# Optimization experiments

Hardware: AMD Instinct MI355X
Metric: run time of the kernel (lower is better)

## Reference

```python
import jax, jax.numpy as jnp
import numpy as np

# config (mirrors init_kwargs)
R = 1.0           # ball-query radius
K = 32            # ball-query neighbors
SPATIAL_STRIDE = 4
TKS = 3           # temporal kernel size (odd)
TPAD = (1, 1)     # replicate temporal padding
HEADS = 8
DIM_HEAD = 64
DIM = 512
MLP = 2048
DEPTH = 2
LN_EPS = 1e-5


def fps(xyz, m):
    # CUDA-style furthest point sampling, starts at index 0. xyz: [N,3] -> [m] int32
    N = xyz.shape[0]
    def body(carry, _):
        dists, last = carry
        d = jnp.sum((xyz - xyz[last]) ** 2, axis=-1)
        dists = jnp.minimum(dists, d)
        nxt = jnp.argmax(dists).astype(jnp.int32)
        return (dists, nxt), nxt
    init = (jnp.full((N,), 1e10, xyz.dtype), jnp.int32(0))
    _, idxs = jax.lax.scan(body, init, None, length=m - 1)
    return jnp.concatenate([jnp.zeros((1,), jnp.int32), idxs])


def ball_query(neighbor_xyz, anchor_xyz):
    # first K neighbor indices within radius R (pad with first found, 0 if none)
    N = neighbor_xyz.shape[0]
    d2 = jnp.sum((anchor_xyz[:, None, :] - neighbor_xyz[None, :, :]) ** 2, -1)  # [M,N]
    cand = jnp.where(d2 < R * R, jnp.arange(N, dtype=jnp.int32)[None, :], N)
    firstk = jnp.sort(cand, axis=-1)[:, :K]
    first = firstk[:, :1]
    idx = jnp.where(firstk >= N, first, firstk)
    return jnp.where(idx >= N, 0, idx).astype(jnp.int32)


def layer_norm(x, g, b):
    mu = jnp.mean(x, -1, keepdims=True)
    var = jnp.var(x, -1, keepdims=True)
    return (x - mu) * jax.lax.rsqrt(var + LN_EPS) * g + b


def p4dconv(xyzs, Wd):
    # tube embedding: FPS anchors + ball-query grouping + 1x1 conv on (dx,dy,dz,dt)
    B, T, N, _ = xyzs.shape
    pad = jnp.concatenate([xyzs[:, :1]] * TPAD[0] + [xyzs] + [xyzs[:, -1:]] * TPAD[1], axis=1)
    Lp = pad.shape[1]
    m = N // SPATIAL_STRIDE
    half = TKS // 2
    new_xyzs, new_feats = [], []
    for t in range(half, Lp - half, 1):  # temporal_stride = 1
        frame = pad[:, t]                                  # [B,N,3]
        aidx = jax.vmap(lambda x: fps(x, m))(frame)        # [B,m]
        anchor = jax.vmap(lambda f, ix: f[ix])(frame, aidx)  # [B,m,3]
        feats_t = []
        for i in range(t - half, t + half + 1):
            nb = pad[:, i]                                 # [B,N,3]
            idx = jax.vmap(ball_query)(nb, anchor)         # [B,m,K]
            grouped = jax.vmap(lambda n, ix: n[ix])(nb, idx)  # [B,m,K,3]
            disp = grouped - anchor[:, :, None, :]
            tdisp = jnp.full((B, m, K, 1), float(i - t), disp.dtype)
            d4 = jnp.concatenate([disp, tdisp], -1)        # [B,m,K,4]
            f = jnp.einsum('bmkf,cf->bmkc', d4, Wd)        # 1x1 conv, no bias/BN/act
            feats_t.append(jnp.max(f, axis=2))             # spatial max pool
        new_feats.append(jnp.max(jnp.stack(feats_t, 1), axis=1))  # temporal max pool
        new_xyzs.append(anchor)
    return jnp.stack(new_xyzs, 1), jnp.stack(new_feats, 1)  # [B,L,m,3], [B,L,m,C]


def attention(xyzs, feats, Wqkv, Wsp, Wout, bout, g, b):
    B, L, n, C = feats.shape
    M = L * n
    x = layer_norm(feats, g, b)
    qkv = jnp.einsum('blnc,ec->blne', x, Wqkv).reshape(B, M, 3, HEADS, DIM_HEAD)
    q, k, v = [jnp.transpose(qkv[:, :, j], (0, 2, 1, 3)) for j in range(3)]  # [B,h,M,d]
    dots = jnp.einsum('bhid,bhjd->bhij', q, k) * (DIM_HEAD ** -0.5)
    attn = jax.nn.softmax(dots, axis=-1)
    out_v = jnp.einsum('bhij,bhjd->bhid', attn, v)
    xyz_f = xyzs.reshape(B, M, 3)
    delta = xyz_f[:, None, :, :] - xyz_f[:, :, None, :]      # [B,i,j,3] = xyz_j - xyz_i
    wdelta = jnp.einsum('bhij,bijc->bhic', attn, delta)      # attn-weighted displacement
    disp_f = jnp.einsum('bhic,dc->bhid', wdelta, Wsp)        # spatial_op Linear(3->d)
    out = out_v + disp_f
    out = jnp.transpose(out, (0, 2, 1, 3)).reshape(B, M, HEADS * DIM_HEAD)
    out = jax.nn.gelu(out @ Wout.T + bout, approximate=False)
    return out.reshape(B, L, n, C) + feats


def feed_forward(x, g, b, W1, b1, W2, b2):
    h = layer_norm(x, g, b)
    h = jax.nn.gelu(h @ W1.T + b1, approximate=False)
    return h @ W2.T + b2 + x


def setup_inputs() -> dict:
    key = jax.random.key(0)
    ks = jax.random.split(key, 12)
    s = 0.02
    inner = HEADS * DIM_HEAD
    return {
        'xyzs': jax.random.normal(ks[0], (2, 4, 1024, 3), jnp.float32),
        'Wd': jax.random.normal(ks[1], (DIM, 4), jnp.float32) * s,
        'Wqkv': jax.random.normal(ks[2], (DEPTH, 3 * inner, DIM), jnp.float32) * s,
        'Wsp': jax.random.normal(ks[3], (DEPTH, DIM_HEAD, 3), jnp.float32) * s,
        'Wout': jax.random.normal(ks[4], (DEPTH, DIM, inner), jnp.float32) * s,
        'bout': jnp.zeros((DEPTH, DIM), jnp.float32),
        'ln1_g': jnp.ones((DEPTH, DIM), jnp.float32),
        'ln1_b': jnp.zeros((DEPTH, DIM), jnp.float32),
        'Wff1': jax.random.normal(ks[5], (DEPTH, MLP, DIM), jnp.float32) * s,
        'bff1': jnp.zeros((DEPTH, MLP), jnp.float32),
        'Wff2': jax.random.normal(ks[6], (DEPTH, DIM, MLP), jnp.float32) * s,
        'bff2': jnp.zeros((DEPTH, DIM), jnp.float32),
        'ln2_g': jnp.ones((DEPTH, DIM), jnp.float32),
        'ln2_b': jnp.zeros((DEPTH, DIM), jnp.float32),
    }


def reference(xyzs, Wd, Wqkv, Wsp, Wout, bout, ln1_g, ln1_b, Wff1, bff1, Wff2, bff2, ln2_g, ln2_b):
    new_xyzs, feats = p4dconv(xyzs, Wd)   # [B,L,m,3], [B,L,m,DIM]
    feats = jax.nn.relu(feats)            # emb_relu after tube embedding
    for i in range(DEPTH):
        feats = attention(new_xyzs, feats, Wqkv[i], Wsp[i], Wout[i], bout[i], ln1_g[i], ln1_b[i])
        feats = feed_forward(feats, ln2_g[i], ln2_b[i], Wff1[i], bff1[i], Wff2[i], bff2[i])
    return feats
```

## Files before the change

kernel.cpp:

```cpp
#include <hip/hip_runtime.h>
#include <math.h>
#include <stdint.h>


typedef __bf16 bf16_t;
typedef __bf16 bf16x8 __attribute__((ext_vector_type(8)));
typedef __bf16 bf16x4 __attribute__((ext_vector_type(4)));
typedef float f32x4 __attribute__((ext_vector_type(4)));

__device__ __forceinline__ void async16(const bf16_t* g, bf16_t* l) {
  __builtin_amdgcn_global_load_lds(
      (const __attribute__((address_space(1))) void*)g,
      (__attribute__((address_space(3))) void*)l, 16, 0, 0);
}

__device__ __forceinline__ float wave_max_dpp(float v) {
  int a = __float_as_int(v);
  int t;
  t = __builtin_amdgcn_update_dpp(a, a, 0x111, 0xf, 0xf, false);
  a = __float_as_int(fmaxf(__int_as_float(a), __int_as_float(t)));
  t = __builtin_amdgcn_update_dpp(a, a, 0x112, 0xf, 0xf, false);
  a = __float_as_int(fmaxf(__int_as_float(a), __int_as_float(t)));
  t = __builtin_amdgcn_update_dpp(a, a, 0x114, 0xf, 0xf, false);
  a = __float_as_int(fmaxf(__int_as_float(a), __int_as_float(t)));
  t = __builtin_amdgcn_update_dpp(a, a, 0x118, 0xf, 0xf, false);
  a = __float_as_int(fmaxf(__int_as_float(a), __int_as_float(t)));
  t = __builtin_amdgcn_update_dpp(a, a, 0x142, 0xf, 0xf, false);
  a = __float_as_int(fmaxf(__int_as_float(a), __int_as_float(t)));
  t = __builtin_amdgcn_update_dpp(a, a, 0x143, 0xf, 0xf, false);
  a = __float_as_int(fmaxf(__int_as_float(a), __int_as_float(t)));
  return __int_as_float(a);
}

template <int CTRL>
__device__ __forceinline__ unsigned long long dpp_max_u64(unsigned long long kv) {
  uint32_t lo = (uint32_t)kv, hi = (uint32_t)(kv >> 32);
  uint32_t lo2 =
      (uint32_t)__builtin_amdgcn_update_dpp((int)lo, (int)lo, CTRL, 0xf, 0xf, false);
  uint32_t hi2 =
      (uint32_t)__builtin_amdgcn_update_dpp((int)hi, (int)hi, CTRL, 0xf, 0xf, false);
  unsigned long long other = ((unsigned long long)hi2 << 32) | lo2;
  return other > kv ? other : kv;
}

__global__ __launch_bounds__(512) void fps_cvt_kernel(
    const float* __restrict__ xyzs, float* __restrict__ anchors,
    const float* __restrict__ s0, bf16_t* __restrict__ d0,
    const float* __restrict__ s1, bf16_t* __restrict__ d1,
    const float* __restrict__ s2, bf16_t* __restrict__ d2,
    const float* __restrict__ s3, bf16_t* __restrict__ d3) {
  int bid = blockIdx.x;
  int tid = threadIdx.x;
  if (bid >= 8) {
    int idx = (bid - 8) * 512 + tid;
    const float* s; bf16_t* d; int off;
    if (idx < 393216) { s = s0; d = d0; off = idx; }
    else if (idx < 524288) { s = s1; d = d1; off = idx - 393216; }
    else if (idx < 1048576) { s = s2; d = d2; off = idx - 524288; }
    else { s = s3; d = d3; off = idx - 1048576; }
    float4 v = ((const float4*)s)[off];
    bf16x4 o = {(bf16_t)v.x, (bf16_t)v.y, (bf16_t)v.z, (bf16_t)v.w};
    ((bf16x4*)d)[off] = o;
    return;
  }
  int to = bid & 3, b = bid >> 2;
  const float* fr = xyzs + (size_t)(b * 4 + to) * 1024 * 3;
  float* an = anchors + (size_t)(b * 4 + to) * 256 * 3;
  __shared__ __align__(16) float4 sp[1024];
  __shared__ __align__(16) unsigned long long keys[2][8];
  int w = tid >> 6, lane = tid & 63;
  float px[2], py[2], pz[2], dist[2];
#pragma unroll
  for (int r = 0; r < 2; ++r) {
    int i = r * 512 + tid;
    float x = fr[i * 3 + 0], y = fr[i * 3 + 1], z = fr[i * 3 + 2];
    px[r] = x; py[r] = y; pz[r] = z; dist[r] = 1e10f;
    sp[i] = make_float4(x, y, z, 0.0f);
  }
  __syncthreads();
  float4 c = sp[0];
  if (tid == 0) { an[0] = c.x; an[1] = c.y; an[2] = c.z; }
  for (int s = 1; s < 256; ++s) {
    int par = s & 1;
#pragma unroll
    for (int r = 0; r < 2; ++r) {
      float dx = px[r] - c.x, dy = py[r] - c.y, dz = pz[r] - c.z;
      float d = fmaf(dx, dx, fmaf(dy, dy, dz * dz));
      dist[r] = fminf(dist[r], d);
    }
    float mloc = fmaxf(dist[0], dist[1]);
    float wmax = wave_max_dpp(mloc);
    float smax = __int_as_float(__builtin_amdgcn_readlane(__float_as_int(wmax), 63));
    unsigned int cidx = 0xFFFFFFFFu;
#pragma unroll
    for (int r = 1; r >= 0; --r) {
      unsigned long long m = __ballot(dist[r] == smax);
      unsigned int tz = (unsigned int)__builtin_ctzll(m | 0x8000000000000000ull);
      unsigned int cand = (unsigned int)(r * 512 + w * 64) + tz;
      cidx = m ? cand : cidx;
    }
    unsigned long long key =
        ((unsigned long long)__float_as_uint(smax) << 32) |
        (unsigned long long)(~cidx);
    if (lane == 0) keys[par][w] = key;
    __syncthreads();
    unsigned long long kv = keys[par][lane & 7];
    kv = dpp_max_u64<0xB1>(kv);
    kv = dpp_max_u64<0x4E>(kv);
    kv = dpp_max_u64<0x124>(kv);
    unsigned int bi = ~(unsigned int)(kv & 0xFFFFFFFFull);
    c = sp[bi];
    if (tid == 0) { an[s * 3 + 0] = c.x; an[s * 3 + 1] = c.y; an[s * 3 + 2] = c.z; }
  }
}

__global__ __launch_bounds__(256) void conv_ln_kernel(
    const float* __restrict__ xyzs, const float* __restrict__ anchors,
    const float* __restrict__ Wd, float* __restrict__ feats,
    bf16_t* __restrict__ xln0, const float* __restrict__ g,
    const float* __restrict__ bt) {
  int bid = blockIdx.x;
  int tid = threadIdx.x;
  int j = bid & 255, to = (bid >> 8) & 3, b = bid >> 10;
  __shared__ float disp[96][4];
  __shared__ int idxbuf[3][32];
  __shared__ float red1[4], red2[4];
  const float* an = anchors + (size_t)((b * 4 + to) * 256 + j) * 3;
  float ax = an[0], ay = an[1], az = an[2];
  int w = tid >> 6, lane = tid & 63;
  if (w < 3) {
    int src = to + w - 1; src = src < 0 ? 0 : (src > 3 ? 3 : src);
    const float* nb = xyzs + (size_t)(b * 4 + src) * 1024 * 3;
    int cnt = 0;
    for (int ch = 0; ch < 16; ++ch) {
      if (cnt >= 32) break;
      int i = ch * 64 + lane;
      float dx = ax - nb[i * 3], dy = ay - nb[i * 3 + 1], dz = az - nb[i * 3 + 2];
      float d2 = dx * dx + dy * dy + dz * dz;
      bool in = d2 < 1.0f;
      unsigned long long mask = __ballot(in);
      if (in) {
        int pos = cnt + (int)__popcll(mask & ((1ull << lane) - 1ull));
        if (pos < 32) idxbuf[w][pos] = i;
      }
      cnt += (int)__popcll(mask);
    }
    if (cnt > 32) cnt = 32;
    if (lane >= cnt && lane < 32) idxbuf[w][lane] = (cnt > 0) ? idxbuf[w][0] : 0;
    if (lane < 32) {
      int ni = idxbuf[w][lane];
      int row = w * 32 + lane;
      disp[row][0] = nb[ni * 3 + 0] - ax;
      disp[row][1] = nb[ni * 3 + 1] - ay;
      disp[row][2] = nb[ni * 3 + 2] - az;
      disp[row][3] = (float)(w - 1);
    }
  }
  __syncthreads();
  int row = (b * 1024) + to * 256 + j;
  const float* wr0 = Wd + tid * 4;
  const float* wr1 = Wd + (tid + 256) * 4;
  float w00 = wr0[0], w01 = wr0[1], w02 = wr0[2], w03 = wr0[3];
  float w10 = wr1[0], w11 = wr1[1], w12 = wr1[2], w13 = wr1[3];
  float mx0 = -1e30f, mx1 = -1e30f;
#pragma unroll 8
  for (int nn = 0; nn < 96; ++nn) {
    float a0 = disp[nn][0], a1 = disp[nn][1], a2 = disp[nn][2], a3 = disp[nn][3];
    mx0 = fmaxf(mx0, a0 * w00 + a1 * w01 + a2 * w02 + a3 * w03);
    mx1 = fmaxf(mx1, a0 * w10 + a1 * w11 + a2 * w12 + a3 * w13);
  }
  float v0 = fmaxf(mx0, 0.0f), v1 = fmaxf(mx1, 0.0f);
  float* fout = feats + (size_t)row * 512;
  fout[tid] = v0;
  fout[tid + 256] = v1;
  float s = v0 + v1;
#pragma unroll
  for (int off = 32; off >= 1; off >>= 1) s += __shfl_xor(s, off, 64);
  if (lane == 0) red1[w] = s;
  __syncthreads();
  float mu = (red1[0] + red1[1] + red1[2] + red1[3]) * (1.0f / 512.0f);
  float dd0 = v0 - mu, dd1 = v1 - mu;
  float q = dd0 * dd0 + dd1 * dd1;
#pragma unroll
  for (int off = 32; off >= 1; off >>= 1) q += __shfl_xor(q, off, 64);
  if (lane == 0) red2[w] = q;
  __syncthreads();
  float var = (red2[0] + red2[1] + red2[2] + red2[3]) * (1.0f / 512.0f);
  float rs = rsqrtf(var + 1e-5f);
  bf16_t* yr = xln0 + (size_t)row * 512;
  yr[tid] = (bf16_t)(dd0 * rs * g[tid] + bt[tid]);
  yr[tid + 256] = (bf16_t)(dd1 * rs * g[tid + 256] + bt[tid + 256]);
}

__global__ __launch_bounds__(256) void ln_kernel(
    const float* __restrict__ x, const float* __restrict__ g,
    const float* __restrict__ bt, bf16_t* __restrict__ y) {
  int row = blockIdx.x;
  int tid = threadIdx.x;
  const float* xr = x + (size_t)row * 512;
  float v0 = xr[tid], v1 = xr[tid + 256];
  float s = v0 + v1;
#pragma unroll
  for (int off = 32; off >= 1; off >>= 1) s += __shfl_xor(s, off, 64);
  __shared__ float red1[4], red2[4];
  int w = tid >> 6, lane = tid & 63;
  if (lane == 0) red1[w] = s;
  __syncthreads();
  float mu = (red1[0] + red1[1] + red1[2] + red1[3]) * (1.0f / 512.0f);
  float d0 = v0 - mu, d1 = v1 - mu;
  float q = d0 * d0 + d1 * d1;
#pragma unroll
  for (int off = 32; off >= 1; off >>= 1) q += __shfl_xor(q, off, 64);
  if (lane == 0) red2[w] = q;
  __syncthreads();
  float var = (red2[0] + red2[1] + red2[2] + red2[3]) * (1.0f / 512.0f);
  float rs = rsqrtf(var + 1e-5f);
  bf16_t* yr = y + (size_t)row * 512;
  yr[tid] = (bf16_t)(d0 * rs * g[tid] + bt[tid]);
  yr[tid + 256] = (bf16_t)(d1 * rs * g[tid + 256] + bt[tid + 256]);
}

template <int BM, int BN, bool GELU, bool BIAS, bool RES, bool OUTBF>
__global__ __launch_bounds__(256) void gemm_bf16(
    const bf16_t* __restrict__ A, const bf16_t* __restrict__ W,
    const float* __restrict__ bias, const float* __restrict__ res,
    void* __restrict__ Cout, int Mn, int Nn, int Kn) {
  constexpr int BK = 64;
  constexpr int WM = BM / 2, WN = BN / 2;
  constexpr int MT = WM / 16, NT = WN / 16;
  constexpr int AIT = (BM * BK / 8) / 256;
  constexpr int BIT = (BN * BK / 8) / 256;
  __shared__ __align__(16) bf16_t As[BM * BK];
  __shared__ __align__(16) bf16_t Bs[BN * BK];
  int tid = threadIdx.x;
  int w = tid >> 6, lane = tid & 63;
  int wr = w >> 1, wc = w & 1;
  int m0 = blockIdx.y * BM, n0 = blockIdx.x * BN;
  int l15 = lane & 15, quad = lane >> 4;
  f32x4 acc[MT][NT] = {};

  const int a_fo = (wr * WM + l15) * BK + quad * 8;
  const int b_fo = (wc * WN + l15) * BK + quad * 8;

  for (int k0 = 0; k0 < Kn; k0 += BK) {
    __syncthreads();
#pragma unroll
    for (int i = 0; i < AIT; ++i) {
      int chunk = i * 256 + tid;
      int row = chunk >> 3, c8 = chunk & 7;
      async16(A + ((size_t)(m0 + row) * Kn + k0 + c8 * 8), As + chunk * 8);
    }
#pragma unroll
    for (int i = 0; i < BIT; ++i) {
      int chunk = i * 256 + tid;
      int row = chunk >> 3, c8 = chunk & 7;
      async16(W + ((size_t)(n0 + row) * Kn + k0 + c8 * 8), Bs + chunk * 8);
    }
    __syncthreads();
#pragma unroll
    for (int ks = 0; ks < 2; ++ks) {
      bf16x8 aF[MT], bF[NT];
#pragma unroll
      for (int mt = 0; mt < MT; ++mt)
        aF[mt] = *(const bf16x8*)&As[a_fo + mt * 16 * BK + ks * 32];
#pragma unroll
      for (int nt = 0; nt < NT; ++nt)
        bF[nt] = *(const bf16x8*)&Bs[b_fo + nt * 16 * BK + ks * 32];
#pragma unroll
      for (int mt = 0; mt < MT; ++mt)
#pragma unroll
        for (int nt = 0; nt < NT; ++nt)
          acc[mt][nt] = __builtin_amdgcn_mfma_f32_16x16x32_bf16(
              aF[mt], bF[nt], acc[mt][nt], 0, 0, 0);
    }
  }
  int rbase = quad * 4;
#pragma unroll
  for (int mt = 0; mt < MT; ++mt) {
#pragma unroll
    for (int reg = 0; reg < 4; ++reg) {
      int r = m0 + wr * WM + mt * 16 + rbase + reg;
      size_t roff = (size_t)r * Nn;
#pragma unroll
      for (int nt = 0; nt < NT; ++nt) {
        int c = n0 + wc * WN + nt * 16 + l15;
        float v = acc[mt][nt][reg];
        if (BIAS) v += bias[c];
        if (GELU) v = v * 0.5f * (1.0f + erff(v * 0.7071067811865475f));
        if (RES) v += res[roff + c];
        if (OUTBF) ((bf16_t*)Cout)[roff + c] = (bf16_t)v;
        else ((float*)Cout)[roff + c] = v;
      }
    }
  }
}

__global__ __launch_bounds__(256) void attn_kernel(
    const bf16_t* __restrict__ qkv, const float* __restrict__ xyzf,
    const float* __restrict__ Wsp, bf16_t* __restrict__ outp) {
  int bid = blockIdx.x;
  int qt = bid & 15, h = (bid >> 4) & 7, b = bid >> 7;
  int tid = threadIdx.x;
  int w = tid >> 6, lane = tid & 63;
  int l15 = lane & 15, quad = lane >> 4;

  __shared__ __align__(16) bf16_t Kb[2][64 * 64];
  __shared__ __align__(16) bf16_t Vt[2][64 * 72];
  __shared__ __align__(16) bf16_t Ps[4][16 * 72];
  __shared__ __align__(16) float4 Xs[2][64];

  const size_t tokbase = (size_t)b * 1024;
  int qbase = qt * 64 + w * 16;

  bf16x8 aQ[2];
  {
    const bf16_t* qp = qkv + (tokbase + qbase + l15) * 1536 + h * 64 + quad * 8;
    aQ[0] = *(const bf16x8*)(qp);
    aQ[1] = *(const bf16x8*)(qp + 32);
  }

  f32x4 oacc[4] = {};
  float lr[4] = {}, pxr[4] = {}, pyr[4] = {}, pzr[4] = {};

  auto stage = [&](int ch, int buf) {
    int j0 = ch * 64;
    int r0 = tid >> 3, seg = tid & 7;
    const bf16_t* g0 = qkv + (tokbase + j0 + r0) * 1536 + 512 + h * 64 + seg * 8;
    async16(g0, Kb[buf] + tid * 8);
    const bf16_t* g1 = qkv + (tokbase + j0 + 32 + r0) * 1536 + 512 + h * 64 + seg * 8;
    async16(g1, Kb[buf] + 2048 + tid * 8);
#pragma unroll
    for (int t = 0; t < 4; ++t) {
      int task = t * 256 + tid;
      int rp = task >> 5, c2 = task & 31;
      const uint32_t* vsrc = (const uint32_t*)(qkv + (tokbase + j0 + 2 * rp) * 1536 +
                                               1024 + h * 64 + 2 * c2);
      uint32_t a = vsrc[0];
      uint32_t bq = vsrc[768];
      uint32_t wlo = (a & 0xffffu) | (bq << 16);
      uint32_t whi = (a >> 16) | (bq & 0xffff0000u);
      uint32_t* vd = (uint32_t*)Vt[buf];
      vd[c2 * 72 + rp] = wlo;
      vd[c2 * 72 + 36 + rp] = whi;
    }
    if (tid < 64) {
      const float* xp = xyzf + (tokbase + j0 + tid) * 3;
      Xs[buf][tid] = make_float4(xp[0], xp[1], xp[2], 0.0f);
    }
  };

  stage(0, 0);
  for (int ch = 0; ch < 16; ++ch) {
    int cur = ch & 1;
    __syncthreads();
    if (ch + 1 < 16) stage(ch + 1, cur ^ 1);
    f32x4 sacc[4] = {};
#pragma unroll
    for (int ks = 0; ks < 2; ++ks)
#pragma unroll
      for (int nt = 0; nt < 4; ++nt) {
        bf16x8 bK = *(const bf16x8*)&Kb[cur][(nt * 16 + l15) * 64 + ks * 32 + quad * 8];
        sacc[nt] = __builtin_amdgcn_mfma_f32_16x16x32_bf16(aQ[ks], bK, sacc[nt], 0, 0, 0);
      }
#pragma unroll
    for (int nt = 0; nt < 4; ++nt) {
      float4 xk = Xs[cur][nt * 16 + l15];
#pragma unroll
      for (int reg = 0; reg < 4; ++reg) {
        float p = __expf(sacc[nt][reg] * 0.125f);
        bf16_t pb = (bf16_t)p;
        float pf = (float)pb;
        Ps[w][(quad * 4 + reg) * 72 + nt * 16 + l15] = pb;
        lr[reg] += pf;
        pxr[reg] = fmaf(pf, xk.x, pxr[reg]);
        pyr[reg] = fmaf(pf, xk.y, pyr[reg]);
        pzr[reg] = fmaf(pf, xk.z, pzr[reg]);
      }
    }
    bf16x8 aP[2];
    aP[0] = *(const bf16x8*)&Ps[w][l15 * 72 + quad * 8];
    aP[1] = *(const bf16x8*)&Ps[w][l15 * 72 + 32 + quad * 8];
#pragma unroll
    for (int ks = 0; ks < 2; ++ks)
#pragma unroll
      for (int ct = 0; ct < 4; ++ct) {
        bf16x8 bV = *(const bf16x8*)&Vt[cur][(ct * 16 + l15) * 72 + ks * 32 + quad * 8];
        oacc[ct] = __builtin_amdgcn_mfma_f32_16x16x32_bf16(aP[ks], bV, oacc[ct], 0, 0, 0);
      }
  }
#pragma unroll
  for (int reg = 0; reg < 4; ++reg) {
#pragma unroll
    for (int off = 1; off <= 8; off <<= 1) {
      lr[reg] += __shfl_xor(lr[reg], off, 64);
      pxr[reg] += __shfl_xor(pxr[reg], off, 64);
      pyr[reg] += __shfl_xor(pyr[reg], off, 64);
      pzr[reg] += __shfl_xor(pzr[reg], off, 64);
    }
  }
#pragma unroll
  for (int reg = 0; reg < 4; ++reg) {
    size_t tok = tokbase + qbase + quad * 4 + reg;
    float inv = 1.0f / lr[reg];
    const float* xqp = xyzf + tok * 3;
    float wd0 = pxr[reg] * inv - xqp[0];
    float wd1 = pyr[reg] * inv - xqp[1];
    float wd2 = pzr[reg] * inv - xqp[2];
#pragma unroll
    for (int ct = 0; ct < 4; ++ct) {
      int c = ct * 16 + l15;
      const float* wr = Wsp + c * 3;
      float dv = wd0 * wr[0] + wd1 * wr[1] + wd2 * wr[2];
      outp[tok * 512 + h * 64 + c] = (bf16_t)(oacc[ct][reg] * inv + dv);
    }
  }
}

extern "C" void kernel_launch(void* const* d_in, const int* in_sizes, int n_in,
                              void* d_out, int out_size, void* d_ws, size_t ws_size,
                              hipStream_t stream) {
  const float* xyzs = (const float*)d_in[0];
  const float* Wd   = (const float*)d_in[1];
  const float* Wqkv = (const float*)d_in[2];
  const float* Wsp  = (const float*)d_in[3];
  const float* Wout = (const float*)d_in[4];
  const float* bout = (const float*)d_in[5];
  const float* ln1g = (const float*)d_in[6];
  const float* ln1b = (const float*)d_in[7];
  const float* Wff1 = (const float*)d_in[8];
  const float* bff1 = (const float*)d_in[9];
  const float* Wff2 = (const float*)d_in[10];
  const float* bff2 = (const float*)d_in[11];
  const float* ln2g = (const float*)d_in[12];
  const float* ln2b = (const float*)d_in[13];
  float* out = (float*)d_out;

  float* ws = (float*)d_ws;
  float* anchors = ws;
  float* featsA  = ws + 8192;
  float* featsB  = featsA + 1048576;
  float* big     = featsB + 1048576;
  bf16_t* bigb   = (bf16_t*)big;
  bf16_t* xlnb   = (bf16_t*)(big + 3145728);
  bf16_t* attob  = xlnb + 1048576;
  bf16_t* wq_b   = attob + 1048576;
  bf16_t* wo_b   = wq_b + 1572864;
  bf16_t* w1_b   = wo_b + 524288;
  bf16_t* w2_b   = w1_b + 2097152;

  fps_cvt_kernel<<<3080, 512, 0, stream>>>(xyzs, anchors, Wqkv, wq_b, Wout, wo_b,
                                           Wff1, w1_b, Wff2, w2_b);
  conv_ln_kernel<<<2048, 256, 0, stream>>>(xyzs, anchors, Wd, featsA, xlnb,
                                           ln1g, ln1b);

  for (int dep = 0; dep < 2; ++dep) {
    if (dep == 1)
      ln_kernel<<<2048, 256, 0, stream>>>(featsA, ln1g + 512, ln1b + 512, xlnb);
    gemm_bf16<64, 128, false, false, false, true><<<dim3(12, 32), 256, 0, stream>>>(
        xlnb, wq_b + (size_t)dep * 786432, nullptr, nullptr, bigb, 2048, 1536, 512);
    attn_kernel<<<256, 256, 0, stream>>>(bigb, anchors, Wsp + dep * 192, attob);
    gemm_bf16<32, 64, true, true, true, false><<<dim3(8, 64), 256, 0, stream>>>(
        attob, wo_b + (size_t)dep * 262144, bout + dep * 512, featsA, featsB,
        2048, 512, 512);
    ln_kernel<<<2048, 256, 0, stream>>>(featsB, ln2g + dep * 512, ln2b + dep * 512, xlnb);
    gemm_bf16<64, 128, true, true, false, true><<<dim3(16, 32), 256, 0, stream>>>(
        xlnb, w1_b + (size_t)dep * 1048576, bff1 + dep * 2048, nullptr, bigb,
        2048, 2048, 512);
    float* dst = (dep == 1) ? out : featsA;
    gemm_bf16<32, 64, false, true, true, false><<<dim3(8, 64), 256, 0, stream>>>(
        bigb, w2_b + (size_t)dep * 1048576, bff2 + dep * 512, featsB, dst,
        2048, 512, 2048);
  }
}
```

Measured before the change: 405.4 us.

## Fold LayerNorm into GEMM epilogues via row statistics and precomputed weight sums

Removes the standalone LayerNorm kernels. The LN gain is folded into the bf16 weights, and per-column sums W·g and W·b are precomputed. The consuming GEMM runs on raw bf16 activations and applies mean and rstd in its epilogue. Row sum and sum-of-squares are gathered in the producing GEMM epilogues with atomics, which also write a bf16 copy. This saves launches and memory passes, but the E[x²]−μ² variance can lose precision, and bf16 inputs are no longer normalized before quantization.

```diff
diff --git a/kernel.cpp b/kernel.cpp
--- a/kernel.cpp
+++ b/kernel.cpp
@@ -48,19 +48,66 @@
     const float* __restrict__ s0, bf16_t* __restrict__ d0,
     const float* __restrict__ s1, bf16_t* __restrict__ d1,
     const float* __restrict__ s2, bf16_t* __restrict__ d2,
-    const float* __restrict__ s3, bf16_t* __restrict__ d3) {
+    const float* __restrict__ s3, bf16_t* __restrict__ d3,
+    const float* __restrict__ ln1g, const float* __restrict__ ln1b,
+    const float* __restrict__ ln2g, const float* __restrict__ ln2b,
+    float* __restrict__ c2cb_q, float* __restrict__ c2cb_f,
+    float* __restrict__ statsZ) {
   int bid = blockIdx.x;
   int tid = threadIdx.x;
+  int w = tid >> 6, lane = tid & 63;
+  if (bid >= 3086) {
+    int wv = (bid - 3086) * 8 + w;
+    const float* Wrow; const float* g; const float* bt; float* outp;
+    if (wv < 3072) {
+      int dep = wv / 1536, n = wv % 1536;
+      Wrow = s0 + ((size_t)dep * 1536 + n) * 512;
+      g = ln1g + dep * 512; bt = ln1b + dep * 512;
+      outp = c2cb_q + (size_t)(dep * 1536 + n) * 2;
+    } else {
+      int v2 = wv - 3072;
+      int dep = v2 / 2048, n = v2 % 2048;
+      Wrow = s2 + ((size_t)dep * 2048 + n) * 512;
+      g = ln2g + dep * 512; bt = ln2b + dep * 512;
+      outp = c2cb_f + (size_t)(dep * 2048 + n) * 2;
+    }
+    float4 wa = ((const float4*)Wrow)[lane * 2], wb = ((const float4*)Wrow)[lane * 2 + 1];
+    float4 ga = ((const float4*)g)[lane * 2], gb = ((const float4*)g)[lane * 2 + 1];
+    float4 ba = ((const float4*)bt)[lane * 2], bb = ((const float4*)bt)[lane * 2 + 1];
+    float c2 = wa.x * ga.x + wa.y * ga.y + wa.z * ga.z + wa.w * ga.w +
+               wb.x * gb.x + wb.y * gb.y + wb.z * gb.z + wb.w * gb.w;
+    float cb = wa.x * ba.x + wa.y * ba.y + wa.z * ba.z + wa.w * ba.w +
+               wb.x * bb.x + wb.y * bb.y + wb.z * bb.z + wb.w * bb.w;
+#pragma unroll
+    for (int off = 32; off >= 1; off >>= 1) {
+      c2 += __shfl_xor(c2, off, 64);
+      cb += __shfl_xor(cb, off, 64);
+    }
+    if (lane == 0) { outp[0] = c2; outp[1] = cb; }
+    return;
+  }
   if (bid >= 8) {
     int idx = (bid - 8) * 512 + tid;
-    const float* s; bf16_t* d; int off;
-    if (idx < 393216) { s = s0; d = d0; off = idx; }
-    else if (idx < 524288) { s = s1; d = d1; off = idx - 393216; }
-    else if (idx < 1048576) { s = s2; d = d2; off = idx - 524288; }
-    else { s = s3; d = d3; off = idx - 1048576; }
-    float4 v = ((const float4*)s)[off];
-    bf16x4 o = {(bf16_t)v.x, (bf16_t)v.y, (bf16_t)v.z, (bf16_t)v.w};
-    ((bf16x4*)d)[off] = o;
+    if (idx < 1572864) {
+      const float* s; bf16_t* d; int off;
+      const float* gsc = nullptr; int c = 0;
+      if (idx < 393216) {
+        s = s0; d = d0; off = idx;
+        gsc = ln1g + ((idx >= 196608) ? 512 : 0); c = (idx * 4) & 511;
+      } else if (idx < 524288) { s = s1; d = d1; off = idx - 393216; }
+      else if (idx < 1048576) {
+        s = s2; d = d2; off = idx - 524288;
+        gsc = ln2g + ((off >= 262144) ? 512 : 0); c = (off * 4) & 511;
+      } else { s = s3; d = d3; off = idx - 1048576; }
+      float4 v = ((const float4*)s)[off];
+      if (gsc) {
+        v.x *= gsc[c]; v.y *= gsc[c + 1]; v.z *= gsc[c + 2]; v.w *= gsc[c + 3];
+      }
+      bf16x4 o = {(bf16_t)v.x, (bf16_t)v.y, (bf16_t)v.z, (bf16_t)v.w};
+      ((bf16x4*)d)[off] = o;
+    } else {
+      ((float4*)statsZ)[idx - 1572864] = make_float4(0.f, 0.f, 0.f, 0.f);
+    }
     return;
   }
   int to = bid & 3, b = bid >> 2;
@@ -68,7 +115,6 @@
   float* an = anchors + (size_t)(b * 4 + to) * 256 * 3;
   __shared__ __align__(16) float4 sp[1024];
   __shared__ __align__(16) unsigned long long keys[2][8];
-  int w = tid >> 6, lane = tid & 63;
   float px[2], py[2], pz[2], dist[2];
 #pragma unroll
   for (int r = 0; r < 2; ++r) {
@@ -114,11 +160,10 @@
   }
 }
 
-__global__ __launch_bounds__(256) void conv_ln_kernel(
+__global__ __launch_bounds__(256) void conv_kernel(
     const float* __restrict__ xyzs, const float* __restrict__ anchors,
     const float* __restrict__ Wd, float* __restrict__ feats,
-    bf16_t* __restrict__ xln0, const float* __restrict__ g,
-    const float* __restrict__ bt) {
+    bf16_t* __restrict__ featsb, float* __restrict__ stA0) {
   int bid = blockIdx.x;
   int tid = threadIdx.x;
   int j = bid & 255, to = (bid >> 8) & 3, b = bid >> 10;
@@ -173,58 +218,31 @@
   float* fout = feats + (size_t)row * 512;
   fout[tid] = v0;
   fout[tid + 256] = v1;
+  featsb[(size_t)row * 512 + tid] = (bf16_t)v0;
+  featsb[(size_t)row * 512 + tid + 256] = (bf16_t)v1;
   float s = v0 + v1;
-#pragma unroll
-  for (int off = 32; off >= 1; off >>= 1) s += __shfl_xor(s, off, 64);
-  if (lane == 0) red1[w] = s;
+  float q = v0 * v0 + v1 * v1;
+#pragma unroll
+  for (int off = 32; off >= 1; off >>= 1) {
+    s += __shfl_xor(s, off, 64);
+    q += __shfl_xor(q, off, 64);
+  }
+  if (lane == 0) { red1[w] = s; red2[w] = q; }
   __syncthreads();
-  float mu = (red1[0] + red1[1] + red1[2] + red1[3]) * (1.0f / 512.0f);
-  float dd0 = v0 - mu, dd1 = v1 - mu;
-  float q = dd0 * dd0 + dd1 * dd1;
-#pragma unroll
-  for (int off = 32; off >= 1; off >>= 1) q += __shfl_xor(q, off, 64);
-  if (lane == 0) red2[w] = q;
-  __syncthreads();
-  float var = (red2[0] + red2[1] + red2[2] + red2[3]) * (1.0f / 512.0f);
-  float rs = rsqrtf(var + 1e-5f);
-  bf16_t* yr = xln0 + (size_t)row * 512;
-  yr[tid] = (bf16_t)(dd0 * rs * g[tid] + bt[tid]);
-  yr[tid + 256] = (bf16_t)(dd1 * rs * g[tid + 256] + bt[tid + 256]);
-}
-
-__global__ __launch_bounds__(256) void ln_kernel(
-    const float* __restrict__ x, const float* __restrict__ g,
-    const float* __restrict__ bt, bf16_t* __restrict__ y) {
-  int row = blockIdx.x;
-  int tid = threadIdx.x;
-  const float* xr = x + (size_t)row * 512;
-  float v0 = xr[tid], v1 = xr[tid + 256];
-  float s = v0 + v1;
-#pragma unroll
-  for (int off = 32; off >= 1; off >>= 1) s += __shfl_xor(s, off, 64);
-  __shared__ float red1[4], red2[4];
-  int w = tid >> 6, lane = tid & 63;
-  if (lane == 0) red1[w] = s;
-  __syncthreads();
-  float mu = (red1[0] + red1[1] + red1[2] + red1[3]) * (1.0f / 512.0f);
-  float d0 = v0 - mu, d1 = v1 - mu;
-  float q = d0 * d0 + d1 * d1;
-#pragma unroll
-  for (int off = 32; off >= 1; off >>= 1) q += __shfl_xor(q, off, 64);
-  if (lane == 0) red2[w] = q;
-  __syncthreads();
-  float var = (red2[0] + red2[1] + red2[2] + red2[3]) * (1.0f / 512.0f);
-  float rs = rsqrtf(var + 1e-5f);
-  bf16_t* yr = y + (size_t)row * 512;
-  yr[tid] = (bf16_t)(d0 * rs * g[tid] + bt[tid]);
-  yr[tid + 256] = (bf16_t)(d1 * rs * g[tid + 256] + bt[tid + 256]);
-}
-
-template <int BM, int BN, bool GELU, bool BIAS, bool RES, bool OUTBF>
+  if (tid == 0) {
+    stA0[2 * row] = red1[0] + red1[1] + red1[2] + red1[3];
+    stA0[2 * row + 1] = red2[0] + red2[1] + red2[2] + red2[3];
+  }
+}
+
+template <int BM, int BN, bool GELU, bool BIAS, bool RES, bool OUTBF,
+          bool LNIN, bool STATS>
 __global__ __launch_bounds__(256) void gemm_bf16(
     const bf16_t* __restrict__ A, const bf16_t* __restrict__ W,
     const float* __restrict__ bias, const float* __restrict__ res,
-    void* __restrict__ Cout, int Mn, int Nn, int Kn) {
+    void* __restrict__ Cout, int Mn, int Nn, int Kn,
+    const float* __restrict__ stats, const float* __restrict__ c2cb,
+    float* __restrict__ statsOut, bf16_t* __restrict__ bcopy) {
   constexpr int BK = 64;
   constexpr int WM = BM / 2, WN = BN / 2;
   constexpr int MT = WM / 16, NT = WN / 16;
@@ -281,15 +299,42 @@
     for (int reg = 0; reg < 4; ++reg) {
       int r = m0 + wr * WM + mt * 16 + rbase + reg;
       size_t roff = (size_t)r * Nn;
+      float mu = 0.f, rs = 0.f;
+      if (LNIN) {
+        float s1 = stats[2 * r], s2 = stats[2 * r + 1];
+        mu = s1 * (1.0f / 512.0f);
+        float var = s2 * (1.0f / 512.0f) - mu * mu;
+        rs = rsqrtf(var + 1e-5f);
+      }
+      float rsum = 0.f, rsq = 0.f;
 #pragma unroll
       for (int nt = 0; nt < NT; ++nt) {
         int c = n0 + wc * WN + nt * 16 + l15;
         float v = acc[mt][nt][reg];
+        if (LNIN) {
+          float cc2 = c2cb[2 * c], ccb = c2cb[2 * c + 1];
+          v = rs * v - rs * mu * cc2 + ccb;
+        }
         if (BIAS) v += bias[c];
         if (GELU) v = v * 0.5f * (1.0f + erff(v * 0.7071067811865475f));
         if (RES) v += res[roff + c];
         if (OUTBF) ((bf16_t*)Cout)[roff + c] = (bf16_t)v;
         else ((float*)Cout)[roff + c] = v;
+        if (STATS) {
+          bcopy[roff + c] = (bf16_t)v;
+          rsum += v; rsq += v * v;
+        }
+      }
+      if (STATS) {
+#pragma unroll
+        for (int off = 1; off <= 8; off <<= 1) {
+          rsum += __shfl_xor(rsum, off, 64);
+          rsq += __shfl_xor(rsq, off, 64);
+        }
+        if (l15 == 0) {
+          atomicAdd(&statsOut[2 * r], rsum);
+          atomicAdd(&statsOut[2 * r + 1], rsq);
+        }
       }
     }
   }
@@ -441,34 +486,52 @@
   float* featsB  = featsA + 1048576;
   float* big     = featsB + 1048576;
   bf16_t* bigb   = (bf16_t*)big;
-  bf16_t* xlnb   = (bf16_t*)(big + 3145728);
-  bf16_t* attob  = xlnb + 1048576;
-  bf16_t* wq_b   = attob + 1048576;
+  bf16_t* featsAb = (bf16_t*)(big + 3145728);
+  bf16_t* attob  = featsAb + 1048576;
+  bf16_t* featsBb = attob + 1048576;
+  bf16_t* wq_b   = featsBb + 1048576;
   bf16_t* wo_b   = wq_b + 1572864;
   bf16_t* w1_b   = wo_b + 524288;
   bf16_t* w2_b   = w1_b + 2097152;
-
-  fps_cvt_kernel<<<3080, 512, 0, stream>>>(xyzs, anchors, Wqkv, wq_b, Wout, wo_b,
-                                           Wff1, w1_b, Wff2, w2_b);
-  conv_ln_kernel<<<2048, 256, 0, stream>>>(xyzs, anchors, Wd, featsA, xlnb,
-                                           ln1g, ln1b);
+  float* stA0    = (float*)(w2_b + 2097152);
+  float* statsZ  = stA0 + 4096;
+  float* stB0    = statsZ;
+  float* stB1    = statsZ + 4096;
+  float* stA1    = statsZ + 8192;
+  float* c2cb_q  = statsZ + 12288;
+  float* c2cb_f  = c2cb_q + 6144;
+
+  fps_cvt_kernel<<<3982, 512, 0, stream>>>(
+      xyzs, anchors, Wqkv, wq_b, Wout, wo_b, Wff1, w1_b, Wff2, w2_b,
+      ln1g, ln1b, ln2g, ln2b, c2cb_q, c2cb_f, statsZ);
+  conv_kernel<<<2048, 256, 0, stream>>>(xyzs, anchors, Wd, featsA, featsAb, stA0);
 
   for (int dep = 0; dep < 2; ++dep) {
-    if (dep == 1)
-      ln_kernel<<<2048, 256, 0, stream>>>(featsA, ln1g + 512, ln1b + 512, xlnb);
-    gemm_bf16<64, 128, false, false, false, true><<<dim3(12, 32), 256, 0, stream>>>(
-        xlnb, wq_b + (size_t)dep * 786432, nullptr, nullptr, bigb, 2048, 1536, 512);
+    const float* stA = dep ? stA1 : stA0;
+    float* stB = dep ? stB1 : stB0;
+    gemm_bf16<64, 128, false, false, false, true, true, false>
+        <<<dim3(12, 32), 256, 0, stream>>>(
+        featsAb, wq_b + (size_t)dep * 786432, nullptr, nullptr, bigb,
+        2048, 1536, 512, stA, c2cb_q + (size_t)dep * 3072, nullptr, nullptr);
     attn_kernel<<<256, 256, 0, stream>>>(bigb, anchors, Wsp + dep * 192, attob);
-    gemm_bf16<32, 64, true, true, true, false><<<dim3(8, 64), 256, 0, stream>>>(
+    gemm_bf16<32, 64, true, true, true, false, false, true>
+        <<<dim3(8, 64), 256, 0, stream>>>(
         attob, wo_b + (size_t)dep * 262144, bout + dep * 512, featsA, featsB,
-        2048, 512, 512);
-    ln_kernel<<<2048, 256, 0, stream>>>(featsB, ln2g + dep * 512, ln2b + dep * 512, xlnb);
-    gemm_bf16<64, 128, true, true, false, true><<<dim3(16, 32), 256, 0, stream>>>(
-        xlnb, w1_b + (size_t)dep * 1048576, bff1 + dep * 2048, nullptr, bigb,
-        2048, 2048, 512);
-    float* dst = (dep == 1) ? out : featsA;
-    gemm_bf16<32, 64, false, true, true, false><<<dim3(8, 64), 256, 0, stream>>>(
-        bigb, w2_b + (size_t)dep * 1048576, bff2 + dep * 512, featsB, dst,
-        2048, 512, 2048);
-  }
-}
+        2048, 512, 512, nullptr, nullptr, stB, featsBb);
+    gemm_bf16<64, 128, true, true, false, true, true, false>
+        <<<dim3(16, 32), 256, 0, stream>>>(
+        featsBb, w1_b + (size_t)dep * 1048576, bff1 + dep * 2048, nullptr, bigb,
+        2048, 2048, 512, stB, c2cb_f + (size_t)dep * 4096, nullptr, nullptr);
+    if (dep == 0) {
+      gemm_bf16<32, 64, false, true, true, false, false, true>
+          <<<dim3(8, 64), 256, 0, stream>>>(
+          bigb, w2_b, bff2, featsB, featsA,
+          2048, 512, 2048, nullptr, nullptr, stA1, featsAb);
+    } else {
+      gemm_bf16<32, 64, false, true, true, false, false, false>
+          <<<dim3(8, 64), 256, 0, stream>>>(
+          bigb, w2_b + 1048576, bff2 + 512, featsB, out,
+          2048, 512, 2048, nullptr, nullptr, nullptr, nullptr);
+    }
+  }
+}
```

Result: no change. 408.6 us (+0.8%).
